# Kernel optimization log

Measured on AMD Instinct MI355X. Metric: run time of the kernel, lower is better.

## Reference

```python
import jax, jax.numpy as jnp
import numpy as np

K_ORDER = 3
GRID_N = 10
GRID_LO, GRID_HI = -2.0, 2.0
LAYERS = [(49, 256), (256, 256), (256, 10)]
NCOEF = GRID_N + K_ORDER  # 13


def mish(x):
    return x * jnp.tanh(jax.nn.softplus(x))


def bspline_basis(x):
    # x: (B, in) -> basis (B, in, GRID_N + K_ORDER)
    h = (GRID_HI - GRID_LO) / GRID_N
    knots = GRID_LO + h * jnp.arange(-K_ORDER, GRID_N + K_ORDER + 1, dtype=x.dtype)  # (G+2k+1,)
    xx = x[..., None]
    B = ((xx >= knots[:-1]) & (xx < knots[1:])).astype(x.dtype)  # degree-0, (B,in,G+2k)
    for d in range(1, K_ORDER + 1):
        left = (xx - knots[: -(d + 1)]) / (knots[d:-1] - knots[: -(d + 1)]) * B[..., :-1]
        right = (knots[d + 1:] - xx) / (knots[d + 1:] - knots[1:-d]) * B[..., 1:]
        B = left + right
    return B  # (B, in, G+k)


def kan_layer(x, coef, scale_base, scale_sp, bias):
    # x: (B,in); coef: (in,out,G+k); scales: (in,out); bias: (out,)
    basis = bspline_basis(x)                                   # (B,in,G+k)
    spline = jnp.einsum('big,iog->bo', basis, coef * scale_sp[..., None])
    base = jnp.einsum('bi,io->bo', mish(x), scale_base)
    return base + spline + bias


def setup_inputs() -> dict:
    key = jax.random.key(0)
    ks = jax.random.split(key, 1 + 4 * len(LAYERS))
    inp = {'x': jax.random.normal(ks[0], (8192, 1, 28, 28), dtype=jnp.float32)}
    i = 1
    for li, (fin, fout) in enumerate(LAYERS, start=1):
        inp[f'coef{li}'] = 0.1 * jax.random.normal(ks[i], (fin, fout, NCOEF), dtype=jnp.float32); i += 1
        inp[f'sb{li}'] = 1.0 + 0.1 * jax.random.normal(ks[i], (fin, fout), dtype=jnp.float32); i += 1
        inp[f'sp{li}'] = 1.0 + 0.1 * jax.random.normal(ks[i], (fin, fout), dtype=jnp.float32); i += 1
        inp[f'b{li}'] = jnp.zeros((fout,), dtype=jnp.float32); i += 1
    return inp


def reference(x, coef1, sb1, sp1, b1, coef2, sb2, sp2, b2, coef3, sb3, sp3, b3):
    B = x.shape[0]
    # avg_pool2d(x, 4): 28x28 -> 7x7
    h = x.reshape(B, 1, 7, 4, 7, 4).mean(axis=(3, 5))
    h = h.reshape(B, 49)
    h = kan_layer(h, coef1, sb1, sp1, b1)
    h = kan_layer(h, coef2, sb2, sp2, b2)
    h = kan_layer(h, coef3, sb3, sp3, b3)
    return jax.nn.log_softmax(h, axis=1)
```

## Files before the change

kernel.cpp:

```cpp
#include <hip/hip_runtime.h>
#include <hip/hip_bf16.h>

typedef __bf16 bf16x8_t __attribute__((ext_vector_type(8)));
typedef float f32x4_t __attribute__((ext_vector_type(4)));
using bf16 = __hip_bfloat16;

#define ASG __attribute__((address_space(1)))
#define ASL __attribute__((address_space(3)))

__device__ __forceinline__ void gld_lds16(const void* g, void* l) {
  __builtin_amdgcn_global_load_lds((ASG void*)const_cast<void*>(g),
                                   (ASL void*)l, 16, 0, 0);
}

__device__ __forceinline__ unsigned short f2bf_bits(float v) {
  __hip_bfloat16 h = __float2bfloat16(v);
  return *reinterpret_cast<unsigned short*>(&h);
}

__device__ __forceinline__ float mish_f(float x) {
  float z = __expf(x);
  float n = z * (z + 2.0f);
  float m = x * n / (n + 2.0f);
  return (x > 10.0f) ? x : m;
}

__device__ __forceinline__ void kan_feats28(bf16* dst, float x) {
  unsigned int* d32 = (unsigned int*)dst;
#pragma unroll
  for (int d = 0; d < 7; ++d) d32[d] = 0u;
  float t = (x + 3.2f) * 2.5f;
  if (t >= 0.0f && t < 16.0f) {
    float tf = floorf(t);
    int c = (int)tf;
    float u = t - tf;
    float um = 1.0f - u;
    float u2 = u * u, u3 = u2 * u;
    const float s6 = 1.0f / 6.0f;
    float w0 = um * um * um * s6;
    float w1 = (3.0f * u3 - 6.0f * u2 + 4.0f) * s6;
    float w2 = (-3.0f * u3 + 3.0f * u2 + 3.0f * u + 1.0f) * s6;
    float w3 = u3 * s6;
    int j0 = c - 3;
    if (j0 >= 0)               dst[j0]     = __float2bfloat16(w0);
    if (j0 >= -1 && j0 <= 11)  dst[j0 + 1] = __float2bfloat16(w1);
    if (j0 >= -2 && j0 <= 10)  dst[j0 + 2] = __float2bfloat16(w2);
    if (j0 <= 9)               dst[j0 + 3] = __float2bfloat16(w3);
  }
  dst[13] = __float2bfloat16(mish_f(x));
}

__global__ __launch_bounds__(256) void prep_all(
    const float* __restrict__ c1, const float* __restrict__ sb1, const float* __restrict__ sp1,
    const float* __restrict__ c2, const float* __restrict__ sb2, const float* __restrict__ sp2,
    const float* __restrict__ c3, const float* __restrict__ sb3, const float* __restrict__ sp3,
    bf16* __restrict__ W1t, bf16* __restrict__ W2f, bf16* __restrict__ W3t) {
  const int b = blockIdx.x, o = threadIdx.x;
  float vals[14];
  if (b < 49) {
    const int i = b;
    const size_t io = (size_t)i * 256 + o;
    const float spv = sp1[io];
#pragma unroll
    for (int r = 0; r < 13; ++r) vals[r] = c1[io * 13 + r] * spv;
    vals[13] = sb1[io];
    unsigned int* dst = (unsigned int*)(W1t + (size_t)o * 704 + i * 14);
#pragma unroll
    for (int d = 0; d < 7; ++d)
      dst[d] = (unsigned int)f2bf_bits(vals[2 * d]) |
               ((unsigned int)f2bf_bits(vals[2 * d + 1]) << 16);
  } else if (b == 49) {
    unsigned int* dst = (unsigned int*)(W1t + (size_t)o * 704 + 686);
#pragma unroll
    for (int d = 0; d < 9; ++d) dst[d] = 0u;
  } else if (b < 306) {
    const int i = b - 50;
    const size_t io = (size_t)i * 256 + o;
    const float spv = sp2[io];
#pragma unroll
    for (int r = 0; r < 13; ++r) vals[r] = c2[io * 13 + r] * spv;
    vals[13] = sb2[io];
    const int ntg = o >> 4, lr = o & 15;
#pragma unroll
    for (int d = 0; d < 7; ++d) {
      const int k2 = i * 14 + 2 * d;
      const int kc = k2 / 224, rem = k2 % 224;
      const int ks = rem / 32, r2 = rem % 32, quad = r2 / 8, el = r2 % 8;
      const size_t off = ((size_t)((kc * 7 + ks) * 16 + ntg)) * 512 + lr * 32 + quad * 8 + el;
      *(unsigned int*)(W2f + off) = (unsigned int)f2bf_bits(vals[2 * d]) |
                                    ((unsigned int)f2bf_bits(vals[2 * d + 1]) << 16);
    }
  } else {
    const int i = b - 306;
    if (o < 10) {
      const size_t io = (size_t)i * 10 + o;
      const float spv = sp3[io];
#pragma unroll
      for (int r = 0; r < 13; ++r) vals[r] = c3[io * 13 + r] * spv;
      vals[13] = sb3[io];
      unsigned int* dst = (unsigned int*)(W3t + (size_t)o * 3584 + i * 14);
#pragma unroll
      for (int d = 0; d < 7; ++d)
        dst[d] = (unsigned int)f2bf_bits(vals[2 * d]) |
                 ((unsigned int)f2bf_bits(vals[2 * d + 1]) << 16);
    } else if (o < 16) {
      unsigned int* dst = (unsigned int*)(W3t + (size_t)o * 3584 + i * 14);
#pragma unroll
      for (int d = 0; d < 7; ++d) dst[d] = 0u;
    }
  }
}

__global__ __launch_bounds__(256) void pool_basis1(const float* __restrict__ x,
                                                   bf16* __restrict__ A1) {
  __shared__ __align__(16) float xs[3136];
  __shared__ __align__(16) bf16 arow[4 * 704];
  const int b4 = blockIdx.x * 4, t = threadIdx.x;
  const float4* xsrc = (const float4*)(x + (size_t)b4 * 784);
  float4* xd = (float4*)xs;
#pragma unroll
  for (int l = t; l < 784; l += 256) xd[l] = xsrc[l];
  __syncthreads();
  if (t < 196) {
    const int img = t / 49, p = t - img * 49;
    const int oh = p / 7, ow = p - oh * 7;
    const float* xi = xs + img * 784;
    float s = 0.f;
#pragma unroll
    for (int r = 0; r < 4; ++r)
#pragma unroll
      for (int c = 0; c < 4; ++c) s += xi[(oh * 4 + r) * 28 + ow * 4 + c];
    kan_feats28(&arow[img * 704 + p * 14], s * (1.0f / 16.0f));
  } else if (t < 232) {
    const int q = t - 196;
    const int img = q / 9, d = q - img * 9;
    ((unsigned int*)(arow + img * 704 + 686))[d] = 0u;
  }
  __syncthreads();
  uint4* dst = (uint4*)(A1 + (size_t)b4 * 704);
  const uint4* src = (const uint4*)arow;
#pragma unroll
  for (int l = t; l < 352; l += 256) dst[l] = src[l];
}

__global__ __launch_bounds__(256) void gemm1s(
    const bf16* __restrict__ A, const bf16* __restrict__ Wt,
    const float* __restrict__ bias, float* __restrict__ H) {
  constexpr int K = 704;
  __shared__ __align__(16) bf16 As[64 * 64];
  __shared__ __align__(16) bf16 Bs[64 * 64];
  const int t = threadIdx.x;
  const int wv = t >> 6, lane = t & 63, quad = lane >> 4, lr = lane & 15;
  const int n0 = blockIdx.x * 64;
  const int m0 = blockIdx.y * 64;
  const int srow0 = lane >> 3;
  const int cg = (lane & 7) ^ srow0;
  const bf16* gA0 = A + (size_t)(m0 + 8 * wv + srow0) * K + cg * 8;
  const bf16* gA1 = A + (size_t)(m0 + 32 + 8 * wv + srow0) * K + cg * 8;
  const bf16* gB0 = Wt + (size_t)(n0 + 8 * wv + srow0) * K + cg * 8;
  const bf16* gB1 = Wt + (size_t)(n0 + 32 + 8 * wv + srow0) * K + cg * 8;
  char* const lA = (char*)As + wv * 1024;
  char* const lB = (char*)Bs + wv * 1024;
  const int wm = (wv & 1) * 32, wn = (wv >> 1) * 32;
  const int swz = lr & 7;
  f32x4_t acc00 = {0.f, 0.f, 0.f, 0.f}, acc01 = acc00, acc10 = acc00, acc11 = acc00;
  for (int k0 = 0; k0 < K; k0 += 64) {
    gld_lds16(gA0 + k0, lA);
    gld_lds16(gA1 + k0, lA + 4096);
    gld_lds16(gB0 + k0, lB);
    gld_lds16(gB1 + k0, lB + 4096);
    __syncthreads();
#pragma unroll
    for (int s = 0; s < 2; ++s) {
      const int co = ((s * 4 + quad) ^ swz) * 16;
      bf16x8_t a0 = *(const bf16x8_t*)((char*)As + (wm + lr) * 128 + co);
      bf16x8_t a1 = *(const bf16x8_t*)((char*)As + (wm + 16 + lr) * 128 + co);
      bf16x8_t b0 = *(const bf16x8_t*)((char*)Bs + (wn + lr) * 128 + co);
      bf16x8_t b1 = *(const bf16x8_t*)((char*)Bs + (wn + 16 + lr) * 128 + co);
      acc00 = __builtin_amdgcn_mfma_f32_16x16x32_bf16(a0, b0, acc00, 0, 0, 0);
      acc01 = __builtin_amdgcn_mfma_f32_16x16x32_bf16(a0, b1, acc01, 0, 0, 0);
      acc10 = __builtin_amdgcn_mfma_f32_16x16x32_bf16(a1, b0, acc10, 0, 0, 0);
      acc11 = __builtin_amdgcn_mfma_f32_16x16x32_bf16(a1, b1, acc11, 0, 0, 0);
    }
    __syncthreads();
  }
  const int cb = n0 + wn + lr;
  const float bn0 = bias[cb], bn1 = bias[cb + 16];
#pragma unroll
  for (int r = 0; r < 4; ++r) {
    const size_t row = (size_t)(m0 + wm + quad * 4 + r);
    H[row * 256 + cb] = acc00[r] + bn0;
    H[row * 256 + cb + 16] = acc01[r] + bn1;
    H[(row + 16) * 256 + cb] = acc10[r] + bn0;
    H[(row + 16) * 256 + cb + 16] = acc11[r] + bn1;
  }
}

__global__ __launch_bounds__(512, 4) void kan_gemm2(
    const float* __restrict__ Hin, const bf16* __restrict__ W2f,
    float* __restrict__ Hp) {
  __shared__ __align__(16) bf16 As[2][64 * 232];
  const int t = threadIdx.x;
  const int w = t >> 6, lane = t & 63, quad = lane >> 4, lr = lane & 15;
  const int m0 = blockIdx.x * 64;
  const int z = blockIdx.y;
  const int ej = t & 15, er0 = (t >> 4) & 31;
  const int foff = lr * 32 + quad * 8;
  f32x4_t acc[4][2];
#pragma unroll
  for (int m = 0; m < 4; ++m) {
    acc[m][0] = (f32x4_t){0.f, 0.f, 0.f, 0.f};
    acc[m][1] = (f32x4_t){0.f, 0.f, 0.f, 0.f};
  }
  const float* hp = Hin + (size_t)(m0 + er0) * 256 + z * 64 + ej;
  kan_feats28(As[0] + er0 * 232 + ej * 14, hp[0]);
  kan_feats28(As[0] + (er0 + 32) * 232 + ej * 14, hp[32 * 256]);
  size_t fb = ((size_t)(z * 28 * 16 + w * 2)) * 512 + foff;
  bf16x8_t bA0 = *(const bf16x8_t*)(W2f + fb);
  bf16x8_t bA1 = *(const bf16x8_t*)(W2f + fb + 512);
  bf16x8_t bB0 = *(const bf16x8_t*)(W2f + fb + 8192);
  bf16x8_t bB1 = *(const bf16x8_t*)(W2f + fb + 8192 + 512);
  fb += 2 * 8192;
#pragma unroll
  for (int kcl = 0; kcl < 4; ++kcl) {
    __syncthreads();
    const bf16* cur = As[kcl & 1];
    bf16* nxt = As[(kcl & 1) ^ 1];
#pragma unroll
    for (int ks = 0; ks < 7; ++ks) {
      bf16x8_t bN0, bN1;
      if (kcl * 7 + ks < 26) {
        bN0 = *(const bf16x8_t*)(W2f + fb);
        bN1 = *(const bf16x8_t*)(W2f + fb + 512);
      } else {
        bN0 = bB0; bN1 = bB1;
      }
#pragma unroll
      for (int m = 0; m < 4; ++m) {
        bf16x8_t a = *(const bf16x8_t*)(cur + (m * 16 + lr) * 232 + ks * 32 + quad * 8);
        acc[m][0] = __builtin_amdgcn_mfma_f32_16x16x32_bf16(a, bA0, acc[m][0], 0, 0, 0);
        acc[m][1] = __builtin_amdgcn_mfma_f32_16x16x32_bf16(a, bA1, acc[m][1], 0, 0, 0);
      }
      bA0 = bB0; bA1 = bB1; bB0 = bN0; bB1 = bN1;
      fb += 8192;
    }
    if (kcl < 3) {
      kan_feats28(nxt + er0 * 232 + ej * 14, hp[(kcl + 1) * 16]);
      kan_feats28(nxt + (er0 + 32) * 232 + ej * 14, hp[32 * 256 + (kcl + 1) * 16]);
    }
  }
  float* Hpz = Hp + (size_t)z * (8192 * 256);
  const int c0 = w * 32 + lr;
#pragma unroll
  for (int m = 0; m < 4; ++m)
#pragma unroll
    for (int r = 0; r < 4; ++r) {
      const size_t row = (size_t)(m0 + m * 16 + quad * 4 + r);
      Hpz[row * 256 + c0] = acc[m][0][r];
      Hpz[row * 256 + c0 + 16] = acc[m][1][r];
    }
}

__global__ __launch_bounds__(256) void kan_gemm3(
    const float* __restrict__ Hp, const float* __restrict__ b2,
    const bf16* __restrict__ Wt, float* __restrict__ part) {
  constexpr int K = 3584;
  __shared__ __align__(16) bf16 As[64 * 232];
  __shared__ __align__(16) bf16 Bs[16 * 256];
  const int t = threadIdx.x;
  const int wv = t >> 6, lane = t & 63, quad = lane >> 4, lr = lane & 15;
  const int m0 = blockIdx.x * 64;
  const int z = blockIdx.y;
  const int ej = t & 15, er0 = t >> 4;
  const int brow_sub = lane >> 5, bslot = lane & 31;
  f32x4_t acc = {0.f, 0.f, 0.f, 0.f};
  for (int kcl = 0; kcl < 2; ++kcl) {
    const int kc = z * 2 + kcl;
#pragma unroll
    for (int n = 0; n < 2; ++n) {
      const int row = wv * 4 + n * 2 + brow_sub;
      int c = bslot ^ (row & 7);
      if (c >= 28) c = 0;
      const bf16* src = Wt + (size_t)row * K + kc * 224 + c * 8;
      gld_lds16(src, (char*)Bs + (wv * 4 + n * 2) * 512);
    }
    const float bc = b2[kc * 16 + ej];
    const float* hp = Hp + (size_t)(m0 + er0) * 256 + kc * 16 + ej;
    bf16* arow = As + er0 * 232 + ej * 14;
#pragma unroll
    for (int e = 0; e < 4; ++e) {
      const size_t idx = (size_t)e * 16 * 256;
      float h = hp[idx] + hp[idx + 2097152] + hp[idx + 4194304] + hp[idx + 6291456] + bc;
      kan_feats28(arow + e * 16 * 232, h);
    }
    __syncthreads();
#pragma unroll
    for (int ks = 0; ks < 7; ++ks) {
      const int coA = ks * 64 + quad * 16;
      const int sb = ((ks * 4 + quad) ^ (lr & 7)) * 16;
      bf16x8_t a = *(const bf16x8_t*)((const char*)As + (wv * 16 + lr) * 464 + coA);
      bf16x8_t b = *(const bf16x8_t*)((const char*)Bs + lr * 512 + sb);
      acc = __builtin_amdgcn_mfma_f32_16x16x32_bf16(a, b, acc, 0, 0, 0);
    }
    __syncthreads();
  }
#pragma unroll
  for (int r = 0; r < 4; ++r)
    part[(size_t)z * 131072 + (size_t)lr * 8192 + (m0 + wv * 16 + quad * 4 + r)] = acc[r];
}

__global__ __launch_bounds__(256) void lsm(const float* __restrict__ part,
                                           const float* __restrict__ b3,
                                           float* __restrict__ out) {
  const int row = blockIdx.x * 256 + threadIdx.x;
  float v[10];
#pragma unroll
  for (int o = 0; o < 10; ++o) {
    float s = b3[o];
#pragma unroll
    for (int kc = 0; kc < 8; ++kc) s += part[(size_t)kc * 131072 + (size_t)o * 8192 + row];
    v[o] = s;
  }
  float m = v[0];
#pragma unroll
  for (int o = 1; o < 10; ++o) m = fmaxf(m, v[o]);
  float se = 0.f;
#pragma unroll
  for (int o = 0; o < 10; ++o) se += expf(v[o] - m);
  const float l = m + logf(se);
#pragma unroll
  for (int o = 0; o < 10; ++o) out[(size_t)row * 10 + o] = v[o] - l;
}

extern "C" void kernel_launch(void* const* d_in, const int* in_sizes, int n_in,
                              void* d_out, int out_size, void* d_ws, size_t ws_size,
                              hipStream_t stream) {
  const float* x = (const float*)d_in[0];
  const float* coef1 = (const float*)d_in[1];
  const float* sb1 = (const float*)d_in[2];
  const float* sp1 = (const float*)d_in[3];
  const float* b1 = (const float*)d_in[4];
  const float* coef2 = (const float*)d_in[5];
  const float* sb2 = (const float*)d_in[6];
  const float* sp2 = (const float*)d_in[7];
  const float* b2 = (const float*)d_in[8];
  const float* coef3 = (const float*)d_in[9];
  const float* sb3 = (const float*)d_in[10];
  const float* sp3 = (const float*)d_in[11];
  const float* b3 = (const float*)d_in[12];
  float* out = (float*)d_out;

  char* ws = (char*)d_ws;
  size_t off = 0;
  bf16* A1 = (bf16*)(ws + off);    off += 11534336;
  bf16* W1t = (bf16*)(ws + off);   off += 360448;
  bf16* W2f = (bf16*)(ws + off);   off += 1835008;
  bf16* W3t = (bf16*)(ws + off);   off += 114688;
  float* H1 = (float*)(ws + off);  off += 8388608;
  float* Hp = (float*)(ws + off);  off += 33554432;
  float* part = (float*)(ws + off); off += 4194304;

  prep_all<<<562, 256, 0, stream>>>(coef1, sb1, sp1, coef2, sb2, sp2,
                                    coef3, sb3, sp3, W1t, W2f, W3t);
  pool_basis1<<<2048, 256, 0, stream>>>(x, A1);
  gemm1s<<<dim3(4, 128), 256, 0, stream>>>(A1, W1t, b1, H1);
  kan_gemm2<<<dim3(128, 4), 512, 0, stream>>>(H1, W2f, Hp);
  kan_gemm3<<<dim3(128, 8), 256, 0, stream>>>(Hp, b2, W3t, part);
  lsm<<<32, 256, 0, stream>>>(part, b3, out);
}
```

Before: 146.2 us.

## Prefetch gemm2 weights four steps ahead; load gemm3 weights in fragment layout directly

kan_gemm2 now keeps a four-slot ring of register-held weight fragments, issuing global loads four k-steps ahead instead of two, to better hide global-memory latency behind the MFMAs. Layer-3 weights are repacked by prep_all into an MFMA-fragment-ordered layout so kan_gemm3 reads its B operand straight from global memory into registers, dropping the LDS staging buffer and one barrier per k-chunk. The deeper prefetch raises register pressure in gemm2, and gemm3 now issues per-wave global loads inside its MFMA loop.

```diff
diff --git a/kernel.cpp b/kernel.cpp
--- a/kernel.cpp
+++ b/kernel.cpp
@@ -54,7 +54,7 @@
     const float* __restrict__ c1, const float* __restrict__ sb1, const float* __restrict__ sp1,
     const float* __restrict__ c2, const float* __restrict__ sb2, const float* __restrict__ sp2,
     const float* __restrict__ c3, const float* __restrict__ sb3, const float* __restrict__ sp3,
-    bf16* __restrict__ W1t, bf16* __restrict__ W2f, bf16* __restrict__ W3t) {
+    bf16* __restrict__ W1t, bf16* __restrict__ W2f, bf16* __restrict__ W3f) {
   const int b = blockIdx.x, o = threadIdx.x;
   float vals[14];
   if (b < 49) {
@@ -98,15 +98,21 @@
 #pragma unroll
       for (int r = 0; r < 13; ++r) vals[r] = c3[io * 13 + r] * spv;
       vals[13] = sb3[io];
-      unsigned int* dst = (unsigned int*)(W3t + (size_t)o * 3584 + i * 14);
-#pragma unroll
-      for (int d = 0; d < 7; ++d)
-        dst[d] = (unsigned int)f2bf_bits(vals[2 * d]) |
-                 ((unsigned int)f2bf_bits(vals[2 * d + 1]) << 16);
+#pragma unroll
+      for (int d = 0; d < 7; ++d) {
+        const int k2 = i * 14 + 2 * d;
+        const int s = k2 >> 5, r2 = k2 & 31;
+        const size_t off = (size_t)s * 512 + o * 32 + (r2 >> 3) * 8 + (r2 & 7);
+        *(unsigned int*)(W3f + off) = (unsigned int)f2bf_bits(vals[2 * d]) |
+                                      ((unsigned int)f2bf_bits(vals[2 * d + 1]) << 16);
+      }
     } else if (o < 16) {
-      unsigned int* dst = (unsigned int*)(W3t + (size_t)o * 3584 + i * 14);
-#pragma unroll
-      for (int d = 0; d < 7; ++d) dst[d] = 0u;
+#pragma unroll
+      for (int d = 0; d < 7; ++d) {
+        const int k2 = i * 14 + 2 * d;
+        const int s = k2 >> 5, r2 = k2 & 31;
+        *(unsigned int*)(W3f + (size_t)s * 512 + o * 32 + (r2 >> 3) * 8 + (r2 & 7)) = 0u;
+      }
     }
   }
 }
@@ -215,12 +221,13 @@
   const float* hp = Hin + (size_t)(m0 + er0) * 256 + z * 64 + ej;
   kan_feats28(As[0] + er0 * 232 + ej * 14, hp[0]);
   kan_feats28(As[0] + (er0 + 32) * 232 + ej * 14, hp[32 * 256]);
-  size_t fb = ((size_t)(z * 28 * 16 + w * 2)) * 512 + foff;
-  bf16x8_t bA0 = *(const bf16x8_t*)(W2f + fb);
-  bf16x8_t bA1 = *(const bf16x8_t*)(W2f + fb + 512);
-  bf16x8_t bB0 = *(const bf16x8_t*)(W2f + fb + 8192);
-  bf16x8_t bB1 = *(const bf16x8_t*)(W2f + fb + 8192 + 512);
-  fb += 2 * 8192;
+  const bf16* wbase = W2f + ((size_t)(z * 28 * 16 + w * 2)) * 512 + foff;
+  bf16x8_t p0[4], p1[4];
+#pragma unroll
+  for (int s = 0; s < 4; ++s) {
+    p0[s] = *(const bf16x8_t*)(wbase + (size_t)s * 8192);
+    p1[s] = *(const bf16x8_t*)(wbase + (size_t)s * 8192 + 512);
+  }
 #pragma unroll
   for (int kcl = 0; kcl < 4; ++kcl) {
     __syncthreads();
@@ -228,21 +235,19 @@
     bf16* nxt = As[(kcl & 1) ^ 1];
 #pragma unroll
     for (int ks = 0; ks < 7; ++ks) {
-      bf16x8_t bN0, bN1;
-      if (kcl * 7 + ks < 26) {
-        bN0 = *(const bf16x8_t*)(W2f + fb);
-        bN1 = *(const bf16x8_t*)(W2f + fb + 512);
-      } else {
-        bN0 = bB0; bN1 = bB1;
+      const int step = kcl * 7 + ks;
+      const int slot = step & 3;
+      bf16x8_t b0 = p0[slot], b1 = p1[slot];
+      if (step + 4 < 28) {
+        p0[slot] = *(const bf16x8_t*)(wbase + (size_t)(step + 4) * 8192);
+        p1[slot] = *(const bf16x8_t*)(wbase + (size_t)(step + 4) * 8192 + 512);
       }
 #pragma unroll
       for (int m = 0; m < 4; ++m) {
         bf16x8_t a = *(const bf16x8_t*)(cur + (m * 16 + lr) * 232 + ks * 32 + quad * 8);
-        acc[m][0] = __builtin_amdgcn_mfma_f32_16x16x32_bf16(a, bA0, acc[m][0], 0, 0, 0);
-        acc[m][1] = __builtin_amdgcn_mfma_f32_16x16x32_bf16(a, bA1, acc[m][1], 0, 0, 0);
+        acc[m][0] = __builtin_amdgcn_mfma_f32_16x16x32_bf16(a, b0, acc[m][0], 0, 0, 0);
+        acc[m][1] = __builtin_amdgcn_mfma_f32_16x16x32_bf16(a, b1, acc[m][1], 0, 0, 0);
       }
-      bA0 = bB0; bA1 = bB1; bB0 = bN0; bB1 = bN1;
-      fb += 8192;
     }
     if (kcl < 3) {
       kan_feats28(nxt + er0 * 232 + ej * 14, hp[(kcl + 1) * 16]);
@@ -263,46 +268,34 @@
 
 __global__ __launch_bounds__(256) void kan_gemm3(
     const float* __restrict__ Hp, const float* __restrict__ b2,
-    const bf16* __restrict__ Wt, float* __restrict__ part) {
-  constexpr int K = 3584;
+    const bf16* __restrict__ W3f, float* __restrict__ part) {
   __shared__ __align__(16) bf16 As[64 * 232];
-  __shared__ __align__(16) bf16 Bs[16 * 256];
   const int t = threadIdx.x;
   const int wv = t >> 6, lane = t & 63, quad = lane >> 4, lr = lane & 15;
   const int m0 = blockIdx.x * 64;
   const int z = blockIdx.y;
   const int ej = t & 15, er0 = t >> 4;
-  const int brow_sub = lane >> 5, bslot = lane & 31;
+  const int foff = lr * 32 + quad * 8;
   f32x4_t acc = {0.f, 0.f, 0.f, 0.f};
+#pragma unroll
   for (int kcl = 0; kcl < 2; ++kcl) {
     const int kc = z * 2 + kcl;
-#pragma unroll
-    for (int n = 0; n < 2; ++n) {
-      const int row = wv * 4 + n * 2 + brow_sub;
-      int c = bslot ^ (row & 7);
-      if (c >= 28) c = 0;
-      const bf16* src = Wt + (size_t)row * K + kc * 224 + c * 8;
-      gld_lds16(src, (char*)Bs + (wv * 4 + n * 2) * 512);
-    }
     const float bc = b2[kc * 16 + ej];
     const float* hp = Hp + (size_t)(m0 + er0) * 256 + kc * 16 + ej;
-    bf16* arow = As + er0 * 232 + ej * 14;
+    if (kcl) __syncthreads();
 #pragma unroll
     for (int e = 0; e < 4; ++e) {
       const size_t idx = (size_t)e * 16 * 256;
       float h = hp[idx] + hp[idx + 2097152] + hp[idx + 4194304] + hp[idx + 6291456] + bc;
-      kan_feats28(arow + e * 16 * 232, h);
+      kan_feats28(As + (er0 + 16 * e) * 232 + ej * 14, h);
     }
     __syncthreads();
 #pragma unroll
     for (int ks = 0; ks < 7; ++ks) {
-      const int coA = ks * 64 + quad * 16;
-      const int sb = ((ks * 4 + quad) ^ (lr & 7)) * 16;
-      bf16x8_t a = *(const bf16x8_t*)((const char*)As + (wv * 16 + lr) * 464 + coA);
-      bf16x8_t b = *(const bf16x8_t*)((const char*)Bs + lr * 512 + sb);
+      bf16x8_t b = *(const bf16x8_t*)(W3f + (size_t)(kc * 7 + ks) * 512 + foff);
+      bf16x8_t a = *(const bf16x8_t*)(As + (wv * 16 + lr) * 232 + ks * 32 + quad * 8);
       acc = __builtin_amdgcn_mfma_f32_16x16x32_bf16(a, b, acc, 0, 0, 0);
     }
-    __syncthreads();
   }
 #pragma unroll
   for (int r = 0; r < 4; ++r)
@@ -355,16 +348,16 @@
   bf16* A1 = (bf16*)(ws + off);    off += 11534336;
   bf16* W1t = (bf16*)(ws + off);   off += 360448;
   bf16* W2f = (bf16*)(ws + off);   off += 1835008;
-  bf16* W3t = (bf16*)(ws + off);   off += 114688;
+  bf16* W3f = (bf16*)(ws + off);   off += 114688;
   float* H1 = (float*)(ws + off);  off += 8388608;
   float* Hp = (float*)(ws + off);  off += 33554432;
   float* part = (float*)(ws + off); off += 4194304;
 
   prep_all<<<562, 256, 0, stream>>>(coef1, sb1, sp1, coef2, sb2, sp2,
-                                    coef3, sb3, sp3, W1t, W2f, W3t);
+                                    coef3, sb3, sp3, W1t, W2f, W3f);
   pool_basis1<<<2048, 256, 0, stream>>>(x, A1);
   gemm1s<<<dim3(4, 128), 256, 0, stream>>>(A1, W1t, b1, H1);
   kan_gemm2<<<dim3(128, 4), 512, 0, stream>>>(H1, W2f, Hp);
-  kan_gemm3<<<dim3(128, 8), 256, 0, stream>>>(Hp, b2, W3t, part);
+  kan_gemm3<<<dim3(128, 8), 256, 0, stream>>>(Hp, b2, W3f, part);
   lsm<<<32, 256, 0, stream>>>(part, b3, out);
 }
```

Result: no change. 146.4 us (+0.2%).
